# Optimization experiments

Hardware: AMD Instinct MI355X
Metric: run time of the kernel (lower is better)

Reference implementation:

```python
import jax, jax.numpy as jnp
import numpy as np

N = 50000          # site nodes
L = 32             # max URL token length
E = 64             # embed_size
H = 128            # hidden_size
E_SIM = 800000     # edges per relation in blocks
E_SUB = 200000     # 'sim' edges classified at the end
NEG = 0.01         # LeakyReLU negative slope

def leaky(x):
    return jnp.where(x >= 0, x, NEG * x)

def lstm_final(x, mask, Wih, Whh, b, reverse):
    # x: [N, L, E], mask: [N, L] bool. Returns packed-sequence final hidden [N, E].
    if reverse:
        x = x[:, ::-1, :]
        mask = mask[:, ::-1]
    h0 = jnp.zeros((x.shape[0], Whh.shape[1]), x.dtype)
    def step(carry, inp):
        h, c = carry
        xt, mt = inp
        g = xt @ Wih.T + h @ Whh.T + b
        i, f, gg, o = jnp.split(g, 4, axis=-1)  # PyTorch gate order i,f,g,o
        cn = jax.nn.sigmoid(f) * c + jax.nn.sigmoid(i) * jnp.tanh(gg)
        hn = jax.nn.sigmoid(o) * jnp.tanh(cn)
        m = mt[:, None]
        return (jnp.where(m, hn, h), jnp.where(m, cn, c)), None
    (h, _), _ = jax.lax.scan(step, (h0, h0), (x.transpose(1, 0, 2), mask.T))
    return h

def graph_conv(h, src, dst, W, b):
    # DGL GraphConv, norm='both': D_dst^{-1/2} A D_src^{-1/2} h W + b  (degrees clamped to >=1)
    n = h.shape[0]
    ones = jnp.ones(src.shape[0], h.dtype)
    out_deg = jnp.clip(jax.ops.segment_sum(ones, src, num_segments=n), 1.0)
    in_deg = jnp.clip(jax.ops.segment_sum(ones, dst, num_segments=n), 1.0)
    feat = h * jax.lax.rsqrt(out_deg)[:, None]
    if W.shape[0] > W.shape[1]:
        feat = feat @ W  # project before gather/scatter when in_dim > out_dim (as DGL does)
        rst = jax.ops.segment_sum(feat[src], dst, num_segments=n)
    else:
        rst = jax.ops.segment_sum(feat[src], dst, num_segments=n) @ W
    return rst * jax.lax.rsqrt(in_deg)[:, None] + b

def setup_inputs():
    key = jax.random.key(0)
    ks = iter(jax.random.split(key, 64))
    def nrm(shape, scale=0.05):
        return jax.random.normal(next(ks), shape, dtype=jnp.float32) * scale
    inp = {}
    inp["inputs_s"] = jax.random.randint(next(ks), (N, L), 0, 128)
    lengths = jax.random.randint(next(ks), (N,), 1, L + 1)
    inp["inputs_sm"] = (jnp.arange(L)[None, :] < lengths[:, None]).astype(jnp.int32)
    inp["inputs_c"] = jax.random.randint(next(ks), (N, 1), 0, 101)
    inp["inputs_co"] = jax.random.randint(next(ks), (N, 1), 0, 92)
    inp["inputs_sl"] = jax.random.randint(next(ks), (N, 1), 0, 6)
    for name, m in [("sim_src", E_SIM), ("sim_dst", E_SIM), ("user_src", E_SIM),
                    ("user_dst", E_SIM), ("esub_src", E_SUB), ("esub_dst", E_SUB)]:
        inp[name] = jax.random.randint(next(ks), (m,), 0, N)
    inp["emb_url"] = nrm((128, E)); inp["emb_cat"] = nrm((101, E))
    inp["emb_country"] = nrm((92, E)); inp["emb_sl"] = nrm((6, E))
    for d in ("f", "b"):
        inp["Wih_" + d] = nrm((4 * E, E)); inp["Whh_" + d] = nrm((4 * E, E))
        inp["b_" + d] = nrm((4 * E,))  # b_ih + b_hh folded into one bias
    inp["fc_W"] = nrm((E, 2 * E)); inp["fc_b"] = nrm((E,))
    for i, din in enumerate([4 * E, H]):
        for rel in ("sim", "user"):
            inp["gcn%d_%s_W" % (i, rel)] = nrm((din, H))
            inp["gcn%d_%s_b" % (i, rel)] = nrm((H,))
    inp["cls_W1"] = nrm((H, 2 * H)); inp["cls_b1"] = nrm((H,))
    inp["bn_g"] = jnp.ones((H,), jnp.float32); inp["bn_b"] = jnp.zeros((H,), jnp.float32)
    inp["cls_W2"] = nrm((2, H)); inp["cls_b2"] = nrm((2,))
    return inp

def reference(inputs_s, inputs_sm, inputs_c, inputs_co, inputs_sl,
              sim_src, sim_dst, user_src, user_dst, esub_src, esub_dst,
              emb_url, emb_cat, emb_country, emb_sl,
              Wih_f, Whh_f, b_f, Wih_b, Whh_b, b_b, fc_W, fc_b,
              gcn0_sim_W, gcn0_sim_b, gcn0_user_W, gcn0_user_b,
              gcn1_sim_W, gcn1_sim_b, gcn1_user_W, gcn1_user_b,
              cls_W1, cls_b1, bn_g, bn_b, cls_W2, cls_b2):
    mask = inputs_sm.astype(bool)
    x = emb_url[inputs_s]                                # [N, L, E]
    hf = lstm_final(x, mask, Wih_f, Whh_f, b_f, False)   # h_n[0]
    hb = lstm_final(x, mask, Wih_b, Whh_b, b_b, True)    # h_n[1]
    h_url = leaky(jnp.concatenate([hf, hb], -1) @ fc_W.T + fc_b)  # dropout = identity (eval)
    h = jnp.concatenate([h_url, emb_cat[inputs_c[:, 0]],
                         emb_country[inputs_co[:, 0]], emb_sl[inputs_sl[:, 0]]], -1)  # [N, 4E]
    layers = [(gcn0_sim_W, gcn0_sim_b, gcn0_user_W, gcn0_user_b),
              (gcn1_sim_W, gcn1_sim_b, gcn1_user_W, gcn1_user_b)]
    for Ws, bs, Wu, bu in layers:  # HeteroGraphConv aggregate='sum'
        h = leaky(graph_conv(h, sim_src, sim_dst, Ws, bs)
                  + graph_conv(h, user_src, user_dst, Wu, bu))
    feat = jnp.concatenate([h[esub_src], h[esub_dst]], -1)  # [E_SUB, 2H]
    z = feat @ cls_W1.T + cls_b1
    z = (z - z.mean(0)) * jax.lax.rsqrt(z.var(0) + 1e-5) * bn_g + bn_b  # BatchNorm1d (batch stats)
    z = jnp.maximum(z, 0.0)
    return z @ cls_W2.T + cls_b2
```

## Files before the change

kernel.cpp:

```cpp
#include <hip/hip_runtime.h>
#include <hip/hip_bf16.h>
#include <stdint.h>

#define N_NODES 50000
#define SEQ_L   32
#define NE_BIG  800000
#define NE_SUB  200000
#define DSTRIDE 64

typedef __hip_bfloat16 bf16;
typedef unsigned short u16;
typedef unsigned int u32;
typedef _Float16 f16;
typedef _Float16 v8h __attribute__((ext_vector_type(8)));
typedef float v4f __attribute__((ext_vector_type(4)));

#if __has_builtin(__builtin_amdgcn_exp2f)
#define EXP2(x) __builtin_amdgcn_exp2f(x)
#else
extern "C" __device__ float __ocml_native_exp2_f32(float);
#define EXP2(x) __ocml_native_exp2_f32(x)
#endif
#define LOG2E  1.4426950408889634f
#define LOG2E2 2.8853900817779268f
#define GCLAMP 43.280851226668902f

__device__ __forceinline__ float b2f(bf16 x) { return __bfloat162float(x); }
__device__ __forceinline__ float leakyf(float v) { return v >= 0.f ? v : 0.01f * v; }
__device__ __forceinline__ u16 f2h_bits(float x) { f16 h = (f16)x; u16 b; __builtin_memcpy(&b, &h, 2); return b; }
__device__ __forceinline__ float h2f(u16 b) { f16 h; __builtin_memcpy(&h, &b, 2); return (float)h; }
__device__ __forceinline__ uint pack2h(float a, float b) { return (uint)f2h_bits(a) | ((uint)f2h_bits(b) << 16); }

__device__ __forceinline__ float ldf(const void* p, int i, int isbf) {
  return isbf ? b2f(((const bf16*)p)[i]) : ((const float*)p)[i];
}

__device__ __forceinline__ int detect_isbf(const u16* __restrict__ u) {
  __shared__ int insane;
  if (threadIdx.x == 0) insane = 0;
  __syncthreads();
  int expo = (u[threadIdx.x * 2] >> 7) & 0xFF;
  if (expo >= 147) atomicAdd(&insane, 1);
  __syncthreads();
  return insane == 0;
}

#define NBUCK   391
#define BSHIFT  7
#define BCAP    3072
#define P1_EPT   32
#define P1_CHUNK (256 * P1_EPT)
#define P1_NCH   ((NE_BIG + P1_CHUNK - 1) / P1_CHUNK)
#define P1_BLOCKS (P1_NCH * 2)

struct PrepArgs {
  const void* Whh_f; const void* Whh_b; const void* fc_W; const void* cls_W1;
  const void* g0sW; const void* g0uW; const void* g1sW; const void* g1uW;
  const void* emb_cat; const void* emb_country; const void* emb_sl;
  const void* fc_b; const void* cls_b1; const void* g0sb; const void* g0ub;
  const void* g1sb; const void* g1ub; const void* bn_g; const void* bn_b;
  const void* cls_W2; const void* cls_b2;
  const void* emb_url; const void* Wih_f; const void* b_f; const void* Wih_b; const void* b_b;
  f16* Whh_h; u16* Bfc; u16* BW1; u16* Bg0; u16* Bg1;
  u16* embc_h; u16* embco_h; u16* embs_h;
  float* fcb; float* b1; float* g0sbP; float* g0ubP; float* g1sbP; float* g1ubP;
  float* bngP; float* bnbP; float* W2P; float* b2P;
  int* dflag;
  float* Xperm;
  const int* sm; int* lens; int* cnt33;
  const int* s0; const int* d0; const int* s1; const int* d1;
  int* cnt4; int* gcur; u32* bucket;
};

__global__ __launch_bounds__(256) void prep_graph_kernel(PrepArgs A) {
  const int bid = blockIdx.x;
  const int t = threadIdx.x;

  __shared__ u32 stage[P1_CHUNK];
  __shared__ int hcnt[NBUCK];
  __shared__ int hstart[NBUCK];
  __shared__ int gbase[NBUCK];
  __shared__ int scanbuf[512];

  if (bid < P1_BLOCKS) {
    const int rel = bid & 1;
    const int chunk = bid >> 1;
    const int* s = rel ? A.s1 : A.s0;
    const int* d = rel ? A.d1 : A.d0;
    int* outdeg = A.cnt4 + (size_t)rel * 2 * N_NODES;
    int* gcur = A.gcur + rel * NBUCK;
    u32* bbuf = A.bucket + (size_t)rel * NBUCK * BCAP;
    const int e0 = chunk * P1_CHUNK;
    const int cn = min(NE_BIG - e0, P1_CHUNK);

    for (int b = t; b < NBUCK; b += 256) hcnt[b] = 0;
    __syncthreads();
#pragma unroll
    for (int k = 0; k < P1_EPT; ++k) {
      int i = t + k * 256;
      if (i < cn) {
        int sv = s[e0 + i], dv = d[e0 + i];
        atomicAdd(&outdeg[sv], 1);
        atomicAdd(&hcnt[dv >> BSHIFT], 1);
      }
    }
    __syncthreads();
    scanbuf[t] = (t < NBUCK) ? hcnt[t] : 0;
    scanbuf[t + 256] = (t + 256 < NBUCK) ? hcnt[t + 256] : 0;
    __syncthreads();
    for (int off = 1; off < 512; off <<= 1) {
      int a0 = (t >= off) ? scanbuf[t - off] : 0;
      int a1 = (t + 256 >= off) ? scanbuf[t + 256 - off] : 0;
      __syncthreads();
      scanbuf[t] += a0;
      scanbuf[t + 256] += a1;
      __syncthreads();
    }
    for (int b = t; b < NBUCK; b += 256) {
      int c = hcnt[b];
      int st = scanbuf[b] - c;
      hstart[b] = st;
      gbase[b] = (c > 0) ? atomicAdd(&gcur[b], c) : 0;
      scanbuf[b] = st;
    }
    __syncthreads();
#pragma unroll
    for (int k = 0; k < P1_EPT; ++k) {
      int i = t + k * 256;
      if (i < cn) {
        int sv = s[e0 + i], dv = d[e0 + i];
        int b = dv >> BSHIFT;
        int pos = atomicAdd(&scanbuf[b], 1);
        stage[pos] = ((u32)b << 23) | ((u32)sv << 7) | (u32)(dv & 127);
      }
    }
    __syncthreads();
    for (int i = t; i < cn; i += 256) {
      u32 r = stage[i];
      int b = r >> 23;
      int o = gbase[b] + (i - hstart[b]);
      if (o < BCAP) bbuf[(size_t)b * BCAP + o] = r;
    }
    return;
  }

  const int b = bid - P1_BLOCKS;

  if (b >= 990) {
    int i = (b - 990) * 256 + t;
    if (i >= N_NODES) return;
    int len = 0;
#pragma unroll
    for (int tt = 0; tt < SEQ_L; ++tt) len += __builtin_nontemporal_load(A.sm + i * SEQ_L + tt);
    A.lens[i] = len;
    atomicAdd(&A.cnt33[len], 1);
    return;
  }

  const int isbf = detect_isbf((const u16*)A.emb_url);
  auto cpy = [&](const void* s, float* d, int n, int boff) {
    int i = (b - boff) * 256 + t;
    if (i < n) d[i] = ldf(s, i, isbf);
  };
  auto cvh = [&](const void* s, u16* d, int n, int boff) {
    int i = (b - boff) * 256 + t;
    if (i < n) d[i] = f2h_bits(ldf(s, i, isbf));
  };
  auto cvhW = [&](const void* s, u16* d, int boff) {
    int i = (b - boff) * 256 + t;
    float sc = ((i >> 12) == 2) ? LOG2E2 : LOG2E;
    d[i] = f2h_bits(ldf(s, i, isbf) * sc);
  };
  auto trh = [&](const void* s, u16* d, int R, int C, int KOFF, int boff) {
    int i = (b - boff) * 256 + t;
    if (i < R * C) { int r = i / C, c = i % C; d[c * 256 + KOFF + r] = f2h_bits(ldf(s, i, isbf)); }
  };
  if      (b <   64) cvhW(A.Whh_f, (u16*)A.Whh_h, 0);
  else if (b <  128) cvhW(A.Whh_b, (u16*)(A.Whh_h + 16384), 64);
  else if (b <  160) cvh(A.fc_W, A.Bfc, 8192, 128);
  else if (b <  288) cvh(A.cls_W1, A.BW1, 32768, 160);
  else if (b <  416) trh(A.g0sW, A.Bg0, 256, 128, 0, 288);
  else if (b <  544) trh(A.g0uW, A.Bg0 + 128 * 256, 256, 128, 0, 416);
  else if (b <  608) trh(A.g1sW, A.Bg1, 128, 128, 0, 544);
  else if (b <  672) trh(A.g1uW, A.Bg1, 128, 128, 128, 608);
  else if (b <  698) cvh(A.emb_cat, A.embc_h, 6464, 672);
  else if (b <  721) cvh(A.emb_country, A.embco_h, 5888, 698);
  else if (b <  723) cvh(A.emb_sl, A.embs_h, 384, 721);
  else if (b <  724) cpy(A.fc_b, A.fcb, 64, 723);
  else if (b <  725) cpy(A.cls_b1, A.b1, 128, 724);
  else if (b <  726) cpy(A.g0sb, A.g0sbP, 128, 725);
  else if (b <  727) cpy(A.g0ub, A.g0ubP, 128, 726);
  else if (b <  728) cpy(A.g1sb, A.g1sbP, 128, 727);
  else if (b <  729) cpy(A.g1ub, A.g1ubP, 128, 728);
  else if (b <  730) cpy(A.bn_g, A.bngP, 128, 729);
  else if (b <  731) cpy(A.bn_b, A.bnbP, 128, 730);
  else if (b <  732) cpy(A.cls_W2, A.W2P, 256, 731);
  else if (b <  733) { cpy(A.cls_b2, A.b2P, 2, 732); if (t == 0) A.dflag[0] = isbf; }
  else if (b <  989) {
    int bb = b - 733;
    int dir = bb >> 7;
    int v = bb & 127;
    const void* Wih = dir ? A.Wih_b : A.Wih_f;
    const void* bias = dir ? A.b_b : A.b_f;
    __shared__ float embL[64];
    if (t < 64) embL[t] = ldf(A.emb_url, v * 64 + t, isbf);
    __syncthreads();
    float acc = ldf(bias, t, isbf);
#pragma unroll 8
    for (int j = 0; j < 64; ++j) acc += embL[j] * ldf(Wih, t * 64 + j, isbf);
    int g = t >> 6, unit = t & 63;
    float sc = (g == 2) ? LOG2E2 : LOG2E;
    A.Xperm[(size_t)dir * 128 * 256 + v * 256 + unit * 4 + g] = acc * sc;
  }
}
#define PG_BLOCKS (P1_BLOCKS + 1186)

__global__ __launch_bounds__(256) void permfill_rsq_kernel(
    const int* __restrict__ lens, const int* __restrict__ cnt33, int* __restrict__ cur33,
    int* __restrict__ perm,
    int* __restrict__ cnt4, float* __restrict__ rsq4,
    const u32* __restrict__ bucket, const int* __restrict__ gcur,
    u16* __restrict__ col0, u16* __restrict__ col1)
{
  const int b = blockIdx.x, t = threadIdx.x;
  __shared__ u16 colL[128 * DSTRIDE];
  __shared__ int curL[128];

  if (b < 196) {
    int i = b * 256 + t;
    if (i >= N_NODES) return;
    int len = lens[i];
    int base = 0;
    for (int l = len + 1; l <= SEQ_L; ++l) base += cnt33[l];
    int p = atomicAdd(&cur33[len], 1);
    perm[base + p] = i;
  } else if (b < 196 + 2 * NBUCK) {
    int k = b - 196;
    int rel = k / NBUCK;
    int bk = k % NBUCK;
    const u32* bb = bucket + ((size_t)rel * NBUCK + bk) * BCAP;
    u16* col = rel ? col1 : col0;
    int cnt = gcur[rel * NBUCK + bk];
    if (cnt > BCAP) cnt = BCAP;
    if (t < 128) curL[t] = 0;
    __syncthreads();
    for (int i = t; i < cnt; i += 256) {
      u32 r = bb[i];
      int dl = r & 127;
      int sv = (r >> 7) & 0xFFFF;
      int p = atomicAdd(&curL[dl], 1);
      if (p < DSTRIDE) colL[dl * DSTRIDE + p] = (u16)sv;
    }
    __syncthreads();
    const int node0 = bk << BSHIFT;
    for (int idx = t; idx < 128 * (DSTRIDE / 2); idx += 256) {
      int row = idx >> 5;
      int node = node0 + row;
      if (node < N_NODES)
        ((uint*)(col + (size_t)node * DSTRIDE))[idx & 31] = ((const uint*)colL)[idx];
    }
    if (t < 128) {
      int node = node0 + t;
      if (node < N_NODES) {
        int c = curL[t];
        cnt4[rel * 2 * N_NODES + N_NODES + node] = c;
        float cc = (c < 1) ? 1.f : (float)c;
        rsq4[rel * 2 * N_NODES + N_NODES + node] = __builtin_amdgcn_rsqf(cc);
      }
    }
  } else {
    int idx = (b - 196 - 2 * NBUCK) * 256 + t;
    int i;
    if (idx < N_NODES) i = idx;
    else if (idx < 2 * N_NODES) i = idx + N_NODES;
    else return;
    int c = cnt4[i]; if (c < 1) c = 1;
    rsq4[i] = __builtin_amdgcn_rsqf((float)c);
  }
}
#define PR_BLOCKS (196 + 2 * NBUCK + 391)

__global__ __launch_bounds__(256, 4) void lstm_mfma_kernel(
    const int* __restrict__ perm, const int* __restrict__ lens,
    const int* __restrict__ toksg,
    const float* __restrict__ Xperm,
    const f16* __restrict__ Whh_h,
    u16* __restrict__ hcat_h,
    int nnodes)
{
  __shared__ __align__(16) f16 H[2][64 * 72];
  __shared__ unsigned char toksA[SEQ_L * 64];
  __shared__ int permL[64];
  __shared__ int lensL[64];
  __shared__ int smax;
  const int tid = threadIdx.x;
  const int w = tid >> 6;
  const int lane = tid & 63;
  const int quad = lane >> 4;
  const int lid = lane & 15;
  const int dir = blockIdx.y;

  if (tid < 64) {
    int gid = blockIdx.x * 64 + tid;
    int node = -1, len = 0;
    if (gid < nnodes) { node = perm[gid]; len = lens[node]; }
    permL[tid] = node; lensL[tid] = len;
  }
  if (tid == 0) smax = 0;
  for (int i = tid; i < 64 * 72; i += 256) { H[0][i] = (f16)0.f; H[1][i] = (f16)0.f; }
  for (int i = tid; i < SEQ_L * 16; i += 256) ((uint*)toksA)[i] = 0u;
  __syncthreads();
  if (tid < 64 && lensL[tid] > 0) atomicMax(&smax, lensL[tid]);
  for (int idx = tid; idx < 64 * SEQ_L; idx += 256) {
    int node = idx >> 5, tp = idx & 31;
    int len = lensL[node];
    if (tp < len) {
      int s = dir ? (len - 1 - tp) : tp;
      toksA[s * 64 + node] = (unsigned char)toksg[(size_t)permL[node] * SEQ_L + tp];
    }
  }
  __syncthreads();
  const int tmax = smax;

  const f16* Wd = Whh_h + (size_t)dir * 256 * 64;
  v8h Bf[4][2];
#pragma unroll
  for (int g = 0; g < 4; ++g)
#pragma unroll
    for (int kf = 0; kf < 2; ++kf)
      Bf[g][kf] = *(const v8h*)(Wd + (g * 64 + w * 16 + lid) * 64 + kf * 32 + quad * 8);

  int lenv[16];
#pragma unroll
  for (int mt = 0; mt < 4; ++mt)
#pragma unroll
    for (int r = 0; r < 4; ++r) lenv[mt * 4 + r] = lensL[mt * 16 + quad * 4 + r];

  float creg[16];
  f16 hreg[16];
#pragma unroll
  for (int i = 0; i < 16; ++i) { creg[i] = 0.f; hreg[i] = (f16)0.f; }

  const float* Xp = Xperm + (size_t)dir * 128 * 256;

  for (int step = 0; step < tmax; ++step) {
    const int rb = step & 1, wb = rb ^ 1;
    const unsigned char* trow = &toksA[step * 64];
#pragma unroll
    for (int mt = 0; mt < 4; ++mt) {
      float4 xr[4];
#pragma unroll
      for (int r = 0; r < 4; ++r) {
        int nd = mt * 16 + quad * 4 + r;
        xr[r] = *(const float4*)(Xp + (size_t)trow[nd] * 256 + (w * 16 + lid) * 4);
      }
      const f16* hb = &H[rb][0];
      int arow = (mt * 16 + lid) * 72 + quad * 8;
      v8h a0 = *(const v8h*)(hb + arow);
      v8h a1 = *(const v8h*)(hb + arow + 32);
      v4f acc[4];
#pragma unroll
      for (int g = 0; g < 4; ++g) {
        v4f a = {0.f, 0.f, 0.f, 0.f};
        a = __builtin_amdgcn_mfma_f32_16x16x32_f16(a0, Bf[g][0], a, 0, 0, 0);
        a = __builtin_amdgcn_mfma_f32_16x16x32_f16(a1, Bf[g][1], a, 0, 0, 0);
        acc[g] = a;
      }
#pragma unroll
      for (int r = 0; r < 4; ++r) {
        int idx = mt * 4 + r;
        int nd = mt * 16 + quad * 4 + r;
        bool act = step < lenv[idx];
        float gi = acc[0][r] + xr[r].x;
        float gf = acc[1][r] + xr[r].y;
        float gG = acc[2][r] + xr[r].z;
        float go = acc[3][r] + xr[r].w;
        float A = EXP2(-gi);
        float B = EXP2(-gf);
        float C = EXP2(-go);
        float D = EXP2(fminf(gG, GCLAMP));
        float sf = __builtin_amdgcn_rcpf(1.f + B);
        float sitg = (D - 1.f) * __builtin_amdgcn_rcpf((1.f + A) * (D + 1.f));
        float cn = sf * creg[idx] + sitg;
        float E = EXP2(fminf(cn * LOG2E2, GCLAMP));
        float hn = (E - 1.f) * __builtin_amdgcn_rcpf((1.f + C) * (E + 1.f));
        if (act) { creg[idx] = cn; hreg[idx] = (f16)hn; }
        H[wb][nd * 72 + w * 16 + lid] = hreg[idx];
      }
    }
    __syncthreads();
  }
#pragma unroll
  for (int mt = 0; mt < 4; ++mt)
#pragma unroll
    for (int r = 0; r < 4; ++r) {
      int nd = mt * 16 + quad * 4 + r;
      int gnode = permL[nd];
      if (gnode >= 0) {
        u16 bits; f16 hv = hreg[mt * 4 + r]; __builtin_memcpy(&bits, &hv, 2);
        hcat_h[(size_t)gnode * 128 + dir * 64 + w * 16 + lid] = bits;
      }
    }
}

template<int K, int COLS, int AMODE, bool LEAKY, int OHS, bool EMB, bool BNS>
__global__ __launch_bounds__(256) void mfma_gemm(
    const u16* __restrict__ Ah,
    const int* __restrict__ esrc, const int* __restrict__ edst, const u16* __restrict__ Fh,
    const u16* __restrict__ B,
    const float* __restrict__ bias, const float* __restrict__ bias2,
    const float* __restrict__ rs0, const float* __restrict__ rs1,
    u16* __restrict__ outh0, u16* __restrict__ outh1,
    const int* __restrict__ ic, const int* __restrict__ ico, const int* __restrict__ isl,
    const u16* __restrict__ ech, const u16* __restrict__ ecoh, const u16* __restrict__ eslh,
    float* __restrict__ bnsums,
    int nrows)
{
  constexpr int AST = K + 8;
  constexpr int ABYTES = 64 * AST * 2;
  constexpr int EBYTES = 64 * 129 * 4;
  constexpr int SBYTES = (ABYTES > EBYTES) ? ABYTES : EBYTES;
  __shared__ __align__(16) char smem[SBYTES];
  u16* As = (u16*)smem;
  float* Es = (float*)smem;
  __shared__ int idxL[128];
  __shared__ float bnred[BNS ? 512 : 1];

  const int tid = threadIdx.x;
  const int w = tid >> 6;
  const int lane = tid & 63;
  const int quad = lane >> 4;
  const int lid = lane & 15;
  const int r0 = blockIdx.x * 64;

  if (AMODE == 2) {
    if (tid < 64) {
      int row = r0 + tid;
      idxL[tid] = (row < nrows) ? esrc[row] : -1;
      idxL[64 + tid] = (row < nrows) ? edst[row] : -1;
    }
    __syncthreads();
    for (int idx = tid; idx < 64 * (K / 8); idx += 256) {
      int rn = idx / (K / 8), seg = idx % (K / 8);
      int half = seg >> 4, k8 = seg & 15;
      int base = idxL[half * 64 + rn];
      uint4 v = {0u, 0u, 0u, 0u};
      if (base >= 0) v = *(const uint4*)(Fh + (size_t)base * 128 + k8 * 8);
      *(uint4*)(As + rn * AST + seg * 8) = v;
    }
  } else {
    for (int idx = tid; idx < 64 * (K / 8); idx += 256) {
      int rn = idx / (K / 8), c8 = idx % (K / 8);
      int row = r0 + rn;
      uint4 v = {0u, 0u, 0u, 0u};
      if (row < nrows) v = *(const uint4*)(Ah + (size_t)row * K + c8 * 8);
      *(uint4*)(As + rn * AST + c8 * 8) = v;
    }
  }
  __syncthreads();

  constexpr int NT = COLS / 16;
  v4f acc[NT];
#pragma unroll
  for (int i = 0; i < NT; ++i) acc[i] = (v4f){0.f, 0.f, 0.f, 0.f};

  for (int kb = 0; kb < K / 32; ++kb) {
    v8h a = *(const v8h*)((const f16*)As + (w * 16 + lid) * AST + kb * 32 + quad * 8);
#pragma unroll
    for (int ct = 0; ct < NT; ++ct) {
      v8h b = *(const v8h*)((const f16*)B + (size_t)(ct * 16 + lid) * K + kb * 32 + quad * 8);
      acc[ct] = __builtin_amdgcn_mfma_f32_16x16x32_f16(a, b, acc[ct], 0, 0, 0);
    }
  }

  constexpr int NH = (COLS > 128) ? 2 : 1;
  constexpr int CH = COLS / NH;
  float bs = 0.f, bs2 = 0.f;
#pragma unroll
  for (int h = 0; h < NH; ++h) {
    __syncthreads();
#pragma unroll
    for (int ct = 0; ct < CH / 16; ++ct) {
      int ctg = h * (CH / 16) + ct;
#pragma unroll
      for (int r = 0; r < 4; ++r)
        Es[(w * 16 + quad * 4 + r) * 129 + ct * 16 + lid] = acc[ctg][r];
    }
    __syncthreads();
    for (int idx = tid; idx < 64 * CH; idx += 256) {
      int rn = idx / CH, c = idx % CH;
      int row = r0 + rn;
      float v = 0.f;
      if (row < nrows) {
        v = Es[rn * 129 + c];
        if (bias) v += bias[h * CH + c];
        if (bias2) v += bias2[h * CH + c];
        if (LEAKY) v = leakyf(v);
        const float* rs = (h == 0) ? rs0 : rs1;
        if (rs) v *= rs[row];
        u16* oh = (h == 0) ? outh0 : outh1;
        oh[(size_t)row * OHS + c] = f2h_bits(v);
      }
      if (BNS) { bs += v; bs2 += v * v; }
    }
  }
  if (BNS) {
    bnred[tid] = bs;
    bnred[256 + tid] = bs2;
    __syncthreads();
    if (tid < 128) {
      atomicAdd(&bnsums[tid], bnred[tid] + bnred[tid + 128]);
      atomicAdd(&bnsums[128 + tid], bnred[256 + tid] + bnred[384 + tid]);
    }
  }
  if (EMB) {
    for (int idx = tid; idx < 64 * 192; idx += 256) {
      int rn = idx / 192, j = idx % 192;
      int row = r0 + rn;
      if (row >= nrows) continue;
      u16 v;
      if (j < 64)       v = ech [ic [row] * 64 + j];
      else if (j < 128) v = ecoh[ico[row] * 64 + (j - 64)];
      else              v = eslh[isl[row] * 64 + (j - 128)];
      outh0[(size_t)row * OHS + 64 + j] = v;
    }
  }
}

__global__ __launch_bounds__(256) void gather_merge0_kernel(
    const u16* __restrict__ colS, const int* __restrict__ cntS, const u16* __restrict__ Ps,
    const u16* __restrict__ colU, const int* __restrict__ cntU, const u16* __restrict__ Pu,
    const float* __restrict__ rsS, const float* __restrict__ rsU,
    const float* __restrict__ bS, const float* __restrict__ bU,
    u16* __restrict__ outh, int nnodes)
{
  int wave = threadIdx.x >> 6;
  int lane = threadIdx.x & 63;
  int node = __builtin_amdgcn_readfirstlane(blockIdx.x * 4 + wave);
  if (node >= nnodes) return;
  const uint* PS2 = (const uint*)Ps;
  const uint* PU2 = (const uint*)Pu;
  float2 aS = make_float2(0.f, 0.f), aU = make_float2(0.f, 0.f);
  {
    const u16* col = colS + (size_t)node * DSTRIDE;
    int cnt = min(cntS[node], DSTRIDE);
    int e = 0;
    for (; e + 4 <= cnt; e += 4) {
      uint v0 = PS2[(size_t)col[e] * 64 + lane];
      uint v1 = PS2[(size_t)col[e + 1] * 64 + lane];
      uint v2 = PS2[(size_t)col[e + 2] * 64 + lane];
      uint v3 = PS2[(size_t)col[e + 3] * 64 + lane];
      aS.x += h2f((u16)v0) + h2f((u16)v1) + h2f((u16)v2) + h2f((u16)v3);
      aS.y += h2f((u16)(v0 >> 16)) + h2f((u16)(v1 >> 16)) + h2f((u16)(v2 >> 16)) + h2f((u16)(v3 >> 16));
    }
    for (; e < cnt; ++e) {
      uint v = PS2[(size_t)col[e] * 64 + lane];
      aS.x += h2f((u16)v); aS.y += h2f((u16)(v >> 16));
    }
  }
  {
    const u16* col = colU + (size_t)node * DSTRIDE;
    int cnt = min(cntU[node], DSTRIDE);
    int e = 0;
    for (; e + 4 <= cnt; e += 4) {
      uint v0 = PU2[(size_t)col[e] * 64 + lane];
      uint v1 = PU2[(size_t)col[e + 1] * 64 + lane];
      uint v2 = PU2[(size_t)col[e + 2] * 64 + lane];
      uint v3 = PU2[(size_t)col[e + 3] * 64 + lane];
      aU.x += h2f((u16)v0) + h2f((u16)v1) + h2f((u16)v2) + h2f((u16)v3);
      aU.y += h2f((u16)(v0 >> 16)) + h2f((u16)(v1 >> 16)) + h2f((u16)(v2 >> 16)) + h2f((u16)(v3 >> 16));
    }
    for (; e < cnt; ++e) {
      uint v = PU2[(size_t)col[e] * 64 + lane];
      aU.x += h2f((u16)v); aU.y += h2f((u16)(v >> 16));
    }
  }
  float rS = rsS[node], rU = rsU[node];
  float2 bsv = ((const float2*)bS)[lane];
  float2 buv = ((const float2*)bU)[lane];
  float o0 = leakyf(aS.x * rS + bsv.x + aU.x * rU + buv.x);
  float o1 = leakyf(aS.y * rS + bsv.y + aU.y * rU + buv.y);
  ((uint*)outh)[(size_t)node * 64 + lane] = pack2h(o0, o1);
}

__global__ __launch_bounds__(256) void gather_cat1_kernel(
    const u16* __restrict__ colS, const int* __restrict__ cntS,
    const u16* __restrict__ colU, const int* __restrict__ cntU,
    const u16* __restrict__ Fh,
    const float* __restrict__ rsoutS, const float* __restrict__ rsoutU,
    const float* __restrict__ rsinS, const float* __restrict__ rsinU,
    u16* __restrict__ Acat, int nnodes)
{
  int wave = threadIdx.x >> 6;
  int lane = threadIdx.x & 63;
  int node = __builtin_amdgcn_readfirstlane(blockIdx.x * 4 + wave);
  if (node >= nnodes) return;
  const uint* F2 = (const uint*)Fh;
  float2 aS = make_float2(0.f, 0.f), aU = make_float2(0.f, 0.f);
  {
    const u16* col = colS + (size_t)node * DSTRIDE;
    int cnt = min(cntS[node], DSTRIDE);
    int e = 0;
    for (; e + 2 <= cnt; e += 2) {
      int s0 = col[e], s1 = col[e + 1];
      float c0 = rsoutS[s0], c1 = rsoutS[s1];
      uint v0 = F2[(size_t)s0 * 64 + lane];
      uint v1 = F2[(size_t)s1 * 64 + lane];
      aS.x += c0 * h2f((u16)v0) + c1 * h2f((u16)v1);
      aS.y += c0 * h2f((u16)(v0 >> 16)) + c1 * h2f((u16)(v1 >> 16));
    }
    for (; e < cnt; ++e) {
      int s = col[e]; float c = rsoutS[s];
      uint v = F2[(size_t)s * 64 + lane];
      aS.x += c * h2f((u16)v); aS.y += c * h2f((u16)(v >> 16));
    }
  }
  {
    const u16* col = colU + (size_t)node * DSTRIDE;
    int cnt = min(cntU[node], DSTRIDE);
    int e = 0;
    for (; e + 2 <= cnt; e += 2) {
      int s0 = col[e], s1 = col[e + 1];
      float c0 = rsoutU[s0], c1 = rsoutU[s1];
      uint v0 = F2[(size_t)s0 * 64 + lane];
      uint v1 = F2[(size_t)s1 * 64 + lane];
      aU.x += c0 * h2f((u16)v0) + c1 * h2f((u16)v1);
      aU.y += c0 * h2f((u16)(v0 >> 16)) + c1 * h2f((u16)(v1 >> 16));
    }
    for (; e < cnt; ++e) {
      int s = col[e]; float c = rsoutU[s];
      uint v = F2[(size_t)s * 64 + lane];
      aU.x += c * h2f((u16)v); aU.y += c * h2f((u16)(v >> 16));
    }
  }
  float rs = rsinS[node], ru = rsinU[node];
  ((uint*)Acat)[(size_t)node * 128 + lane] = pack2h(aS.x * rs, aS.y * rs);
  ((uint*)Acat)[(size_t)node * 128 + 64 + lane] = pack2h(aU.x * ru, aU.y * ru);
}

__global__ __launch_bounds__(256) void out_kernel(
    const u16* __restrict__ zh, const float* __restrict__ bnsums,
    const float* __restrict__ g, const float* __restrict__ bb, float M,
    const float* __restrict__ W2, const float* __restrict__ b2,
    void* __restrict__ out, int Mi, const int* __restrict__ flag)
{
  __shared__ float lds[128 * 65];
  __shared__ float red[64 * 8];
  __shared__ float ssL[256];
  const int tid = threadIdx.x;
  const int n = tid & 63;
  const int q = __builtin_amdgcn_readfirstlane(tid >> 6);
  const int r0 = blockIdx.x * 64;
  if (tid < 128) {
    float mean = bnsums[tid] / M;
    float var = bnsums[128 + tid] / M - mean * mean;
    float sc = g[tid] * __builtin_amdgcn_rsqf(var + 1e-5f);
    ssL[tid] = sc;
    ssL[128 + tid] = bb[tid] - mean * sc;
  }
  for (int idx = tid; idx < 64 * 128; idx += 256) {
    int rn = idx >> 7, j = idx & 127;
    int row = r0 + rn;
    lds[j * 65 + rn] = (row < Mi) ? h2f(zh[(size_t)row * 128 + j]) : 0.f;
  }
  __syncthreads();
  float a0 = 0.f, a1 = 0.f;
#pragma unroll 8
  for (int jj = 0; jj < 32; ++jj) {
    int j = q * 32 + jj;
    float y = lds[j * 65 + n] * ssL[j] + ssL[128 + j];
    y = y > 0.f ? y : 0.f;
    a0 += y * W2[j];
    a1 += y * W2[128 + j];
  }
  red[n * 8 + q * 2 + 0] = a0;
  red[n * 8 + q * 2 + 1] = a1;
  __syncthreads();
  if (q == 0 && (r0 + n) < Mi) {
    float o0 = red[n * 8] + red[n * 8 + 2] + red[n * 8 + 4] + red[n * 8 + 6] + b2[0];
    float o1 = red[n * 8 + 1] + red[n * 8 + 3] + red[n * 8 + 5] + red[n * 8 + 7] + b2[1];
    size_t oi = (size_t)(r0 + n) * 2;
    if (*flag) {
      ((bf16*)out)[oi + 0] = __float2bfloat16(o0);
      ((bf16*)out)[oi + 1] = __float2bfloat16(o1);
    } else {
      ((float*)out)[oi + 0] = o0;
      ((float*)out)[oi + 1] = o1;
    }
  }
}

extern "C" void kernel_launch(void* const* d_in, const int* in_sizes, int n_in,
                              void* d_out, int out_size, void* d_ws, size_t ws_size,
                              hipStream_t stream) {
  (void)in_sizes; (void)n_in; (void)out_size; (void)ws_size;
  const int N = N_NODES;
  const int* inputs_s  = (const int*)d_in[0];
  const int* inputs_sm = (const int*)d_in[1];
  const int* inputs_c  = (const int*)d_in[2];
  const int* inputs_co = (const int*)d_in[3];
  const int* inputs_sl = (const int*)d_in[4];
  const int* sim_src   = (const int*)d_in[5];
  const int* sim_dst   = (const int*)d_in[6];
  const int* user_src  = (const int*)d_in[7];
  const int* user_dst  = (const int*)d_in[8];
  const int* esub_src  = (const int*)d_in[9];
  const int* esub_dst  = (const int*)d_in[10];

  char* base = (char*)d_ws;
  size_t off = 0;
  auto alloc = [&](size_t bytes) -> char* {
    char* p = base + off;
    off += (bytes + 255) & ~(size_t)255;
    return p;
  };
  int* dflag    = (int*)alloc(256);
  f16* Whh_h    = (f16*)alloc(2 * 256 * 64 * 2);
  float* Xperm  = (float*)alloc(2 * 128 * 256 * 4);
  u16* Bfc      = (u16*)alloc(64 * 128 * 2);
  u16* BW1      = (u16*)alloc(128 * 256 * 2);
  u16* Bg0      = (u16*)alloc(256 * 256 * 2);
  u16* Bg1      = (u16*)alloc(128 * 256 * 2);
  u16* P_embc_h = (u16*)alloc(6464 * 2);
  u16* P_embco_h= (u16*)alloc(5888 * 2);
  u16* P_embs_h = (u16*)alloc(384 * 2);
  float* P_fcb  = (float*)alloc(64 * 4);
  float* P_b1   = (float*)alloc(128 * 4);
  float* P_g0sb = (float*)alloc(128 * 4);
  float* P_g0ub = (float*)alloc(128 * 4);
  float* P_g1sb = (float*)alloc(128 * 4);
  float* P_g1ub = (float*)alloc(128 * 4);
  float* P_bng  = (float*)alloc(128 * 4);
  float* P_bnb  = (float*)alloc(128 * 4);
  float* P_W2   = (float*)alloc(256 * 4);
  float* P_b2   = (float*)alloc(2 * 4);
  int* lens     = (int*)alloc((size_t)N * 4);
  int* perm     = (int*)alloc((size_t)N * 4);
  float* rsq4   = (float*)alloc((size_t)4 * N * 4);
  char* zbase   = alloc((size_t)4 * N * 4 + 4864);
  int* cnt4     = (int*)zbase;
  int* cnt33    = (int*)(zbase + (size_t)4 * N * 4);
  int* cur33    = cnt33 + 64;
  float* bnsums = (float*)(zbase + (size_t)4 * N * 4 + 512);
  int* gcur     = (int*)(zbase + (size_t)4 * N * 4 + 1536);
  const size_t zbytes = (size_t)4 * N * 4 + 4864;
  char* bufA = alloc((size_t)N * 256 * 4);
  char* bufB = alloc((size_t)N * 256 * 2);
  char* bufC = alloc((size_t)N * 256 * 2);
  char* bufE = alloc((size_t)N * 128 * 2);
  u16* h_h     = (u16*)bufA;
  u16* zh      = (u16*)bufA;
  u16* col_sim = (u16*)(bufA + (size_t)N * 256 * 2);
  u16* col_usr = (u16*)(bufA + (size_t)N * 256 * 2 + (size_t)N * DSTRIDE * 2);
  u16* hcat_h = (u16*)bufB;
  u16* h1_h   = (u16*)bufB;
  u32* bucket = (u32*)bufC;
  u16* Ps_h   = (u16*)bufC;
  u16* Pu_h   = Ps_h + (size_t)N * 128;
  u16* Acat   = (u16*)bufC;
  u16* F_h    = (u16*)bufE;

  const int NB64 = (N + 63) / 64;
  const int NBZ  = (NE_SUB + 63) / 64;

  hipMemsetAsync(zbase, 0, zbytes, stream);

  PrepArgs PA;
  PA.Whh_f = d_in[16]; PA.Whh_b = d_in[19]; PA.fc_W = d_in[21]; PA.cls_W1 = d_in[31];
  PA.g0sW = d_in[23]; PA.g0uW = d_in[25]; PA.g1sW = d_in[27]; PA.g1uW = d_in[29];
  PA.emb_cat = d_in[12]; PA.emb_country = d_in[13]; PA.emb_sl = d_in[14];
  PA.fc_b = d_in[22]; PA.cls_b1 = d_in[32]; PA.g0sb = d_in[24]; PA.g0ub = d_in[26];
  PA.g1sb = d_in[28]; PA.g1ub = d_in[30]; PA.bn_g = d_in[33]; PA.bn_b = d_in[34];
  PA.cls_W2 = d_in[35]; PA.cls_b2 = d_in[36];
  PA.emb_url = d_in[11]; PA.Wih_f = d_in[15]; PA.b_f = d_in[17]; PA.Wih_b = d_in[18]; PA.b_b = d_in[20];
  PA.Whh_h = Whh_h; PA.Bfc = Bfc; PA.BW1 = BW1; PA.Bg0 = Bg0; PA.Bg1 = Bg1;
  PA.embc_h = P_embc_h; PA.embco_h = P_embco_h; PA.embs_h = P_embs_h;
  PA.fcb = P_fcb; PA.b1 = P_b1; PA.g0sbP = P_g0sb; PA.g0ubP = P_g0ub; PA.g1sbP = P_g1sb; PA.g1ubP = P_g1ub;
  PA.bngP = P_bng; PA.bnbP = P_bnb; PA.W2P = P_W2; PA.b2P = P_b2;
  PA.dflag = dflag; PA.Xperm = Xperm;
  PA.sm = inputs_sm; PA.lens = lens; PA.cnt33 = cnt33;
  PA.s0 = sim_src; PA.d0 = sim_dst; PA.s1 = user_src; PA.d1 = user_dst;
  PA.cnt4 = cnt4; PA.gcur = gcur; PA.bucket = bucket;
  prep_graph_kernel<<<PG_BLOCKS, 256, 0, stream>>>(PA);

  permfill_rsq_kernel<<<PR_BLOCKS, 256, 0, stream>>>(lens, cnt33, cur33, perm, cnt4, rsq4,
                                                     bucket, gcur, col_sim, col_usr);

  lstm_mfma_kernel<<<dim3(NB64, 2), 256, 0, stream>>>(perm, lens, inputs_s, Xperm, Whh_h, hcat_h, N);

  mfma_gemm<128, 64, 1, true, 256, true, false><<<NB64, 256, 0, stream>>>(
      hcat_h, nullptr, nullptr, nullptr, Bfc, P_fcb, nullptr, nullptr, nullptr,
      h_h, nullptr, inputs_c, inputs_co, inputs_sl, P_embc_h, P_embco_h, P_embs_h, nullptr, N);

  mfma_gemm<256, 256, 1, false, 128, false, false><<<NB64, 256, 0, stream>>>(
      h_h, nullptr, nullptr, nullptr, Bg0, nullptr, nullptr, rsq4, rsq4 + 2 * N,
      Ps_h, Pu_h, nullptr, nullptr, nullptr, nullptr, nullptr, nullptr, nullptr, N);

  gather_merge0_kernel<<<(N + 3) / 4, 256, 0, stream>>>(col_sim, cnt4 + N, Ps_h,
                                                        col_usr, cnt4 + 3 * N, Pu_h,
                                                        rsq4 + N, rsq4 + 3 * N, P_g0sb, P_g0ub, h1_h, N);

  gather_cat1_kernel<<<(N + 3) / 4, 256, 0, stream>>>(col_sim, cnt4 + N, col_usr, cnt4 + 3 * N, h1_h,
                                                      rsq4, rsq4 + 2 * N, rsq4 + N, rsq4 + 3 * N, Acat, N);

  mfma_gemm<256, 128, 1, true, 128, false, false><<<NB64, 256, 0, stream>>>(
      Acat, nullptr, nullptr, nullptr, Bg1, P_g1sb, P_g1ub, nullptr, nullptr,
      F_h, nullptr, nullptr, nullptr, nullptr, nullptr, nullptr, nullptr, nullptr, N);

  mfma_gemm<256, 128, 2, false, 128, false, true><<<NBZ, 256, 0, stream>>>(
      nullptr, esub_src, esub_dst, F_h, BW1, P_b1, nullptr, nullptr, nullptr,
      zh, nullptr, nullptr, nullptr, nullptr, nullptr, nullptr, nullptr, bnsums, NE_SUB);

  out_kernel<<<NBZ, 256, 0, stream>>>(zh, bnsums, P_bng, P_bnb, (float)NE_SUB,
                                      P_W2, P_b2, d_out, NE_SUB, dflag);
}
```

Before: 1.104 ms.

## Process 128 sorted sequences per LSTM block with prefix-count activity masks

```diff
diff --git a/kernel.cpp b/kernel.cpp
--- a/kernel.cpp
+++ b/kernel.cpp
@@ -280,7 +280,7 @@
 }
 #define PR_BLOCKS (196 + 2 * NBUCK + 391)
 
-__global__ __launch_bounds__(256, 4) void lstm_mfma_kernel(
+__global__ __launch_bounds__(256, 3) void lstm_mfma_kernel(
     const int* __restrict__ perm, const int* __restrict__ lens,
     const int* __restrict__ toksg,
     const float* __restrict__ Xperm,
@@ -288,11 +288,11 @@
     u16* __restrict__ hcat_h,
     int nnodes)
 {
-  __shared__ __align__(16) f16 H[2][64 * 72];
-  __shared__ unsigned char toksA[SEQ_L * 64];
-  __shared__ int permL[64];
-  __shared__ int lensL[64];
-  __shared__ int smax;
+  __shared__ __align__(16) f16 H[2][128 * 72];
+  __shared__ unsigned char toksA[SEQ_L * 128];
+  __shared__ int permL[128];
+  __shared__ int lensL[128];
+  __shared__ int cutL[SEQ_L + 1];
   const int tid = threadIdx.x;
   const int w = tid >> 6;
   const int lane = tid & 63;
@@ -300,27 +300,34 @@
   const int lid = lane & 15;
   const int dir = blockIdx.y;
 
-  if (tid < 64) {
-    int gid = blockIdx.x * 64 + tid;
+  if (tid < 128) {
+    int gid = blockIdx.x * 128 + tid;
     int node = -1, len = 0;
     if (gid < nnodes) { node = perm[gid]; len = lens[node]; }
     permL[tid] = node; lensL[tid] = len;
   }
-  if (tid == 0) smax = 0;
-  for (int i = tid; i < 64 * 72; i += 256) { H[0][i] = (f16)0.f; H[1][i] = (f16)0.f; }
-  for (int i = tid; i < SEQ_L * 16; i += 256) ((uint*)toksA)[i] = 0u;
+  {
+    uint* Hz = (uint*)&H[0][0];
+    for (int i = tid; i < 2 * 128 * 72 / 2; i += 256) Hz[i] = 0u;
+    for (int i = tid; i < SEQ_L * 32; i += 256) ((uint*)toksA)[i] = 0u;
+  }
   __syncthreads();
-  if (tid < 64 && lensL[tid] > 0) atomicMax(&smax, lensL[tid]);
-  for (int idx = tid; idx < 64 * SEQ_L; idx += 256) {
+  if (tid <= SEQ_L) {
+    int c = 0;
+#pragma unroll 8
+    for (int n = 0; n < 128; ++n) c += (lensL[n] > tid) ? 1 : 0;
+    cutL[tid] = c;
+  }
+  for (int idx = tid; idx < 128 * SEQ_L; idx += 256) {
     int node = idx >> 5, tp = idx & 31;
     int len = lensL[node];
     if (tp < len) {
       int s = dir ? (len - 1 - tp) : tp;
-      toksA[s * 64 + node] = (unsigned char)toksg[(size_t)permL[node] * SEQ_L + tp];
+      toksA[s * 128 + node] = (unsigned char)toksg[(size_t)permL[node] * SEQ_L + tp];
     }
   }
   __syncthreads();
-  const int tmax = smax;
+  const int tmax = lensL[0];
 
   const f16* Wd = Whh_h + (size_t)dir * 256 * 64;
   v8h Bf[4][2];
@@ -330,51 +337,50 @@
     for (int kf = 0; kf < 2; ++kf)
       Bf[g][kf] = *(const v8h*)(Wd + (g * 64 + w * 16 + lid) * 64 + kf * 32 + quad * 8);
 
-  int lenv[16];
-#pragma unroll
-  for (int mt = 0; mt < 4; ++mt)
-#pragma unroll
-    for (int r = 0; r < 4; ++r) lenv[mt * 4 + r] = lensL[mt * 16 + quad * 4 + r];
-
-  float creg[16];
-  f16 hreg[16];
-#pragma unroll
-  for (int i = 0; i < 16; ++i) { creg[i] = 0.f; hreg[i] = (f16)0.f; }
-
-  const float* Xp = Xperm + (size_t)dir * 128 * 256;
+  float creg[32];
+  f16 hreg[32];
+#pragma unroll
+  for (int i = 0; i < 32; ++i) { creg[i] = 0.f; hreg[i] = (f16)0.f; }
+
+  const char* Xp = (const char*)(Xperm + (size_t)dir * 128 * 256);
+  const uint xlane = (uint)((w * 16 + lid) * 16);
 
   for (int step = 0; step < tmax; ++step) {
     const int rb = step & 1, wb = rb ^ 1;
-    const unsigned char* trow = &toksA[step * 64];
-#pragma unroll
-    for (int mt = 0; mt < 4; ++mt) {
+    const int cut = cutL[step];
+    const unsigned char* trow = &toksA[step * 128];
+#pragma unroll
+    for (int mt = 0; mt < 8; ++mt) {
       float4 xr[4];
 #pragma unroll
       for (int r = 0; r < 4; ++r) {
         int nd = mt * 16 + quad * 4 + r;
-        xr[r] = *(const float4*)(Xp + (size_t)trow[nd] * 256 + (w * 16 + lid) * 4);
+        uint off = ((uint)trow[nd] << 10) + xlane;
+        xr[r] = *(const float4*)(Xp + off);
       }
       const f16* hb = &H[rb][0];
       int arow = (mt * 16 + lid) * 72 + quad * 8;
       v8h a0 = *(const v8h*)(hb + arow);
       v8h a1 = *(const v8h*)(hb + arow + 32);
       v4f acc[4];
+      acc[0] = (v4f){xr[0].x, xr[1].x, xr[2].x, xr[3].x};
+      acc[1] = (v4f){xr[0].y, xr[1].y, xr[2].y, xr[3].y};
+      acc[2] = (v4f){xr[0].z, xr[1].z, xr[2].z, xr[3].z};
+      acc[3] = (v4f){xr[0].w, xr[1].w, xr[2].w, xr[3].w};
 #pragma unroll
       for (int g = 0; g < 4; ++g) {
-        v4f a = {0.f, 0.f, 0.f, 0.f};
-        a = __builtin_amdgcn_mfma_f32_16x16x32_f16(a0, Bf[g][0], a, 0, 0, 0);
-        a = __builtin_amdgcn_mfma_f32_16x16x32_f16(a1, Bf[g][1], a, 0, 0, 0);
-        acc[g] = a;
+        acc[g] = __builtin_amdgcn_mfma_f32_16x16x32_f16(a0, Bf[g][0], acc[g], 0, 0, 0);
+        acc[g] = __builtin_amdgcn_mfma_f32_16x16x32_f16(a1, Bf[g][1], acc[g], 0, 0, 0);
       }
 #pragma unroll
       for (int r = 0; r < 4; ++r) {
         int idx = mt * 4 + r;
         int nd = mt * 16 + quad * 4 + r;
-        bool act = step < lenv[idx];
-        float gi = acc[0][r] + xr[r].x;
-        float gf = acc[1][r] + xr[r].y;
-        float gG = acc[2][r] + xr[r].z;
-        float go = acc[3][r] + xr[r].w;
+        bool act = nd < cut;
+        float gi = acc[0][r];
+        float gf = acc[1][r];
+        float gG = acc[2][r];
+        float go = acc[3][r];
         float A = EXP2(-gi);
         float B = EXP2(-gf);
         float C = EXP2(-go);
@@ -391,7 +397,7 @@
     __syncthreads();
   }
 #pragma unroll
-  for (int mt = 0; mt < 4; ++mt)
+  for (int mt = 0; mt < 8; ++mt)
 #pragma unroll
     for (int r = 0; r < 4; ++r) {
       int nd = mt * 16 + quad * 4 + r;
@@ -761,6 +767,7 @@
   u16* F_h    = (u16*)bufE;
 
   const int NB64 = (N + 63) / 64;
+  const int NB128 = (N + 127) / 128;
   const int NBZ  = (NE_SUB + 63) / 64;
 
   hipMemsetAsync(zbase, 0, zbytes, stream);
@@ -786,7 +793,7 @@
   permfill_rsq_kernel<<<PR_BLOCKS, 256, 0, stream>>>(lens, cnt33, cur33, perm, cnt4, rsq4,
                                                      bucket, gcur, col_sim, col_usr);
 
-  lstm_mfma_kernel<<<dim3(NB64, 2), 256, 0, stream>>>(perm, lens, inputs_s, Xperm, Whh_h, hcat_h, N);
+  lstm_mfma_kernel<<<dim3(NB128, 2), 256, 0, stream>>>(perm, lens, inputs_s, Xperm, Whh_h, hcat_h, N);
 
   mfma_gemm<128, 64, 1, true, 256, true, false><<<NB64, 256, 0, stream>>>(
       hcat_h, nullptr, nullptr, nullptr, Bfc, P_fcb, nullptr, nullptr, nullptr,
```

Result: slower. 1.133 ms (+2.6%).
